# Optimization experiments

Hardware: AMD Instinct MI355X
Metric: run time of the kernel (lower is better)

## Reference

```python
import jax, jax.numpy as jnp
import numpy as np

N_NODES = 100000
N_EDGES = 640000
IN_DIM = 64
HID = 128
NUM_GRAPHS = 128
MPNN_STEPS = 3
S2S_STEPS = 3


def setup_inputs() -> dict:
    key = jax.random.key(0)
    ks = jax.random.split(key, 20)
    x = jax.random.normal(ks[0], (N_NODES, IN_DIM), dtype=jnp.float32)
    edge_index = jax.random.randint(ks[1], (2, N_EDGES), 0, N_NODES, dtype=jnp.int32)
    batch = jnp.sort(jax.random.randint(ks[2], (N_NODES,), 0, NUM_GRAPHS, dtype=jnp.int32))
    s = 1.0 / np.sqrt(HID)
    params = {
        # input layer Linear(64 -> 128)
        'W_in': jax.random.normal(ks[3], (HID, IN_DIM), dtype=jnp.float32) * s,
        'b_in': jax.random.normal(ks[4], (HID,), dtype=jnp.float32) * s,
        # MGU parameters (torch.randn init in source)
        'W_f': jax.random.normal(ks[5], (HID, HID), dtype=jnp.float32),
        'U_f': jax.random.normal(ks[6], (HID, HID), dtype=jnp.float32),
        'b_f': jax.random.normal(ks[7], (HID,), dtype=jnp.float32),
        'W_h': jax.random.normal(ks[8], (HID, HID), dtype=jnp.float32),
        'U_h': jax.random.normal(ks[9], (HID, HID), dtype=jnp.float32),
        'b_h': jax.random.normal(ks[10], (HID,), dtype=jnp.float32),
        # Set2Set LSTM: input 2*HID, hidden HID, gate order i,f,g,o
        'lstm_w_ih': jax.random.normal(ks[11], (4 * HID, 2 * HID), dtype=jnp.float32) * s,
        'lstm_w_hh': jax.random.normal(ks[12], (4 * HID, HID), dtype=jnp.float32) * s,
        'lstm_b_ih': jax.random.normal(ks[13], (4 * HID,), dtype=jnp.float32) * s,
        'lstm_b_hh': jax.random.normal(ks[14], (4 * HID,), dtype=jnp.float32) * s,
        # prediction layer Linear(2*HID -> 1)
        'W_pred': jax.random.normal(ks[15], (1, 2 * HID), dtype=jnp.float32) * s,
        'b_pred': jax.random.normal(ks[16], (1,), dtype=jnp.float32) * s,
    }
    return {'x': x, 'edge_index': edge_index, 'batch': batch, **params}


def _mpnn_mgu(h, src, dst, W_f, U_f, b_f, W_h, U_h, b_h):
    # sum-aggregate neighbor messages: m_i = sum_{j->i} h_j
    m = jax.ops.segment_sum(h[src], dst, num_segments=N_NODES)  # [N, H]
    f_t = jax.nn.sigmoid(m @ W_f.T + h @ U_f.T + b_f)
    h_hat = jnp.tanh(m @ W_h.T + (f_t * h) @ U_h.T + b_h)
    return (1.0 - f_t) * h + f_t * h_hat


def _set2set(x, batch, w_ih, w_hh, b_ih, b_hh):
    G, H = NUM_GRAPHS, HID
    q_star = jnp.zeros((G, 2 * H), dtype=x.dtype)
    h_l = jnp.zeros((G, H), dtype=x.dtype)
    c_l = jnp.zeros((G, H), dtype=x.dtype)
    for _ in range(S2S_STEPS):
        gates = q_star @ w_ih.T + h_l @ w_hh.T + b_ih + b_hh  # [G, 4H]
        i, f, g, o = jnp.split(gates, 4, axis=-1)
        c_l = jax.nn.sigmoid(f) * c_l + jax.nn.sigmoid(i) * jnp.tanh(g)
        h_l = jax.nn.sigmoid(o) * jnp.tanh(c_l)
        q = h_l  # [G, H]
        # attention over nodes within each graph segment
        e = jnp.sum(x * q[batch], axis=-1)  # [N]
        e_max = jax.ops.segment_max(e, batch, num_segments=G)
        a_un = jnp.exp(e - e_max[batch])
        denom = jax.ops.segment_sum(a_un, batch, num_segments=G)
        a = a_un / denom[batch]
        r = jax.ops.segment_sum(a[:, None] * x, batch, num_segments=G)  # [G, H]
        q_star = jnp.concatenate([q, r], axis=-1)
    return q_star


def reference(x, edge_index, batch, W_in, b_in, W_f, U_f, b_f, W_h, U_h, b_h,
              lstm_w_ih, lstm_w_hh, lstm_b_ih, lstm_b_hh, W_pred, b_pred):
    h = jax.nn.relu(x @ W_in.T + b_in)  # [N, HID]
    src, dst = edge_index[0], edge_index[1]
    for _ in range(MPNN_STEPS):
        h = _mpnn_mgu(h, src, dst, W_f, U_f, b_f, W_h, U_h, b_h)
    q_star = _set2set(h, batch, lstm_w_ih, lstm_w_hh, lstm_b_ih, lstm_b_hh)  # [G, 2H]
    return q_star @ W_pred.T + b_pred  # [G, 1]
```

## Files before the change

### kernel.cpp

```cpp
#include <hip/hip_runtime.h>
#include <math.h>

#define N_NODES 100000
#define N_EDGES 640000
#define IN_DIM 64
#define HID 128
#define NGRAPH 128

typedef __bf16 bf16x2 __attribute__((ext_vector_type(2)));
typedef __bf16 bf16x4 __attribute__((ext_vector_type(4)));
typedef __bf16 bf16x8 __attribute__((ext_vector_type(8)));
typedef float f32x4 __attribute__((ext_vector_type(4)));

#define LDST 136
#define KCAT 384
#define KPAD 392

__device__ __forceinline__ float sigmoid_f(float z) {
  return __fdividef(1.f, 1.f + __expf(-z));
}
__device__ __forceinline__ float tanh_f(float z) {
  return 1.f - __fdividef(2.f, __expf(2.f * z) + 1.f);
}

__device__ __forceinline__ void fma44(const float4 A[4], const float4 B[4], float acc[4][4]) {
#pragma unroll
  for (int i2 = 0; i2 < 4; ++i2) {
    acc[i2][0] += A[i2].x*B[0].x + A[i2].y*B[1].x + A[i2].z*B[2].x + A[i2].w*B[3].x;
    acc[i2][1] += A[i2].x*B[0].y + A[i2].y*B[1].y + A[i2].z*B[2].y + A[i2].w*B[3].y;
    acc[i2][2] += A[i2].x*B[0].z + A[i2].y*B[1].z + A[i2].z*B[2].z + A[i2].w*B[3].z;
    acc[i2][3] += A[i2].x*B[0].w + A[i2].y*B[1].w + A[i2].z*B[2].w + A[i2].w*B[3].w;
  }
}

__global__ __launch_bounds__(256) void k_input(const float* __restrict__ x,
                                               const float* __restrict__ W,
                                               const float* __restrict__ b,
                                               float* __restrict__ h) {
  __shared__ float wS[64][132];
  __shared__ float xS[32][68];
  int t = threadIdx.x;
  int nb = blockIdx.x * 32;
#pragma unroll
  for (int i = 0; i < 8; ++i) {
    int idx4 = i * 256 + t;
    int j = idx4 >> 4, kq = idx4 & 15;
    float4 v = ((const float4*)W)[j * 16 + kq];
    wS[4*kq+0][j] = v.x; wS[4*kq+1][j] = v.y; wS[4*kq+2][j] = v.z; wS[4*kq+3][j] = v.w;
  }
#pragma unroll
  for (int i = 0; i < 2; ++i) {
    int idx4 = i * 256 + t;
    int n = idx4 >> 4, kq = idx4 & 15;
    float4 v = ((const float4*)x)[(nb + n) * 16 + kq];
    *((float4*)&xS[n][4*kq]) = v;
  }
  __syncthreads();
  int bq = t & 31, a = t >> 5;
  float acc[4][4] = {};
#pragma unroll
  for (int kk4 = 0; kk4 < 16; ++kk4) {
    float4 A[4], B[4];
#pragma unroll
    for (int i2 = 0; i2 < 4; ++i2) A[i2] = *((const float4*)&xS[4*a+i2][4*kk4]);
#pragma unroll
    for (int c = 0; c < 4; ++c) B[c] = *((const float4*)&wS[4*kk4+c][4*bq]);
    fma44(A, B, acc);
  }
  float4 bb = ((const float4*)b)[bq];
  float ba[4] = {bb.x, bb.y, bb.z, bb.w};
#pragma unroll
  for (int i2 = 0; i2 < 4; ++i2) {
    float4 o;
    o.x = fmaxf(acc[i2][0] + ba[0], 0.f);
    o.y = fmaxf(acc[i2][1] + ba[1], 0.f);
    o.z = fmaxf(acc[i2][2] + ba[2], 0.f);
    o.w = fmaxf(acc[i2][3] + ba[3], 0.f);
    ((float4*)h)[(nb + 4*a + i2) * 32 + bq] = o;
  }
}

__global__ __launch_bounds__(256) void k_hist(const int* __restrict__ dst,
                                              int* __restrict__ deg) {
  int e = blockIdx.x * 256 + threadIdx.x;
  if (e < N_EDGES) atomicAdd(&deg[dst[e]], 1);
}

#define SCAN_CHUNK 4096
#define SCAN_NB 25

__global__ __launch_bounds__(256) void k_scan_part(const int* __restrict__ deg,
                                                   int* __restrict__ bsum) {
  __shared__ int red[256];
  int t = threadIdx.x, b = blockIdx.x;
  int base = b * SCAN_CHUNK + t * 16;
  int s = 0;
#pragma unroll
  for (int i = 0; i < 16; ++i) {
    int idx = base + i;
    if (idx < N_NODES) s += deg[idx];
  }
  red[t] = s;
  __syncthreads();
  for (int off = 128; off > 0; off >>= 1) {
    if (t < off) red[t] += red[t + off];
    __syncthreads();
  }
  if (t == 0) bsum[b] = red[0];
}

__global__ void k_scan_mid(const int* __restrict__ bsum, int* __restrict__ boff,
                           int* __restrict__ rowstart) {
  if (threadIdx.x == 0) {
    int run = 0;
    for (int i = 0; i < SCAN_NB; ++i) { boff[i] = run; run += bsum[i]; }
    rowstart[N_NODES] = run;
  }
}

__global__ __launch_bounds__(256) void k_scan_final(const int* __restrict__ deg,
                                                    const int* __restrict__ boff,
                                                    int* __restrict__ rowstart) {
  __shared__ int ts[256];
  int t = threadIdx.x, b = blockIdx.x;
  int base = b * SCAN_CHUNK + t * 16;
  int v[16];
  int s = 0;
#pragma unroll
  for (int i = 0; i < 16; ++i) {
    int idx = base + i;
    v[i] = (idx < N_NODES) ? deg[idx] : 0;
    s += v[i];
  }
  ts[t] = s;
  __syncthreads();
  for (int off = 1; off < 256; off <<= 1) {
    int add = (t >= off) ? ts[t - off] : 0;
    __syncthreads();
    ts[t] += add;
    __syncthreads();
  }
  int run = boff[b] + ts[t] - s;
#pragma unroll
  for (int i = 0; i < 16; ++i) {
    int idx = base + i;
    if (idx < N_NODES) rowstart[idx] = run;
    run += v[i];
  }
}

__global__ __launch_bounds__(256) void k_fill(const int* __restrict__ src,
                                              const int* __restrict__ dst,
                                              int* __restrict__ cursor,
                                              int* __restrict__ srcSorted) {
  int e = blockIdx.x * 256 + threadIdx.x;
  if (e >= N_EDGES) return;
  int d = dst[e];
  int p = atomicAdd(&cursor[d], 1);
  srcSorted[p] = src[e];
}

__global__ __launch_bounds__(256) void k_wsplit(const float* __restrict__ W0,
                                                const float* __restrict__ W1,
                                                const float* __restrict__ W2,
                                                const float* __restrict__ W3,
                                                __bf16* __restrict__ Whi,
                                                __bf16* __restrict__ Wlo) {
  int id = blockIdx.x * 256 + threadIdx.x;
  int mat = id >> 14, idx = id & 16383;
  const float* W = (mat == 0) ? W0 : (mat == 1) ? W1 : (mat == 2) ? W2 : W3;
  float v = W[idx];
  __bf16 hi = (__bf16)v;
  Whi[id] = hi;
  Wlo[id] = (__bf16)(v - (float)hi);
}

__global__ void k_wsplit2(const float* __restrict__ w_ih,
                          const float* __restrict__ w_hh,
                          __bf16* __restrict__ WcHi,
                          __bf16* __restrict__ WcLo) {
  int j = blockIdx.x;
  int k = threadIdx.x;
  float v = (k < 256) ? w_ih[j * 256 + k] : w_hh[j * 128 + (k - 256)];
  __bf16 hi = (__bf16)v;
  WcHi[j * KCAT + k] = hi;
  WcLo[j * KCAT + k] = (__bf16)(v - (float)hi);
}

__global__ __launch_bounds__(256) void k_gather(const float* __restrict__ h,
                                                const int* __restrict__ rowstart,
                                                const int* __restrict__ srcSorted,
                                                float* __restrict__ m) {
  int node = blockIdx.x * 8 + (threadIdx.x >> 5);
  if (node >= N_NODES) return;
  int li = threadIdx.x & 31;
  int j0 = rowstart[node], j1 = rowstart[node + 1];
  const float4* h4 = (const float4*)h;
  float4 a0 = {0.f, 0.f, 0.f, 0.f}, a1 = {0.f, 0.f, 0.f, 0.f};
  int j = j0;
  for (; j + 1 < j1; j += 2) {
    int s0 = srcSorted[j], s1 = srcSorted[j + 1];
    float4 v0 = h4[s0 * 32 + li];
    float4 v1 = h4[s1 * 32 + li];
    a0.x += v0.x; a0.y += v0.y; a0.z += v0.z; a0.w += v0.w;
    a1.x += v1.x; a1.y += v1.y; a1.z += v1.z; a1.w += v1.w;
  }
  if (j < j1) {
    int s0 = srcSorted[j];
    float4 v0 = h4[s0 * 32 + li];
    a0.x += v0.x; a0.y += v0.y; a0.z += v0.z; a0.w += v0.w;
  }
  float4 o = {a0.x + a1.x, a0.y + a1.y, a0.z + a1.z, a0.w + a1.w};
  ((float4*)m)[node * 32 + li] = o;
}

__global__ __launch_bounds__(256) void k_mgu(float* __restrict__ h,
                                             const float* __restrict__ m,
                                             const __bf16* __restrict__ Whi,
                                             const __bf16* __restrict__ Wlo,
                                             const float* __restrict__ bfp,
                                             const float* __restrict__ bhp) {
  __shared__ __bf16 mHi[64 * LDST], mLo[64 * LDST];
  __shared__ __bf16 hHi[64 * LDST], hLo[64 * LDST];
  const int t = threadIdx.x;
  const int nb = blockIdx.x * 64;

#pragma unroll
  for (int i = 0; i < 8; ++i) {
    int idx4 = i * 256 + t;
    int n = idx4 >> 5, kq = idx4 & 31;
    float4 vm = ((const float4*)m)[(nb + n) * 32 + kq];
    float4 vh = ((const float4*)h)[(nb + n) * 32 + kq];
    bf16x4 mh, ml, hh, hl;
    mh[0] = (__bf16)vm.x; ml[0] = (__bf16)(vm.x - (float)mh[0]);
    mh[1] = (__bf16)vm.y; ml[1] = (__bf16)(vm.y - (float)mh[1]);
    mh[2] = (__bf16)vm.z; ml[2] = (__bf16)(vm.z - (float)mh[2]);
    mh[3] = (__bf16)vm.w; ml[3] = (__bf16)(vm.w - (float)mh[3]);
    hh[0] = (__bf16)vh.x; hl[0] = (__bf16)(vh.x - (float)hh[0]);
    hh[1] = (__bf16)vh.y; hl[1] = (__bf16)(vh.y - (float)hh[1]);
    hh[2] = (__bf16)vh.z; hl[2] = (__bf16)(vh.z - (float)hh[2]);
    hh[3] = (__bf16)vh.w; hl[3] = (__bf16)(vh.w - (float)hh[3]);
    int e0 = n * LDST + 4 * kq;
    *(bf16x4*)&mHi[e0] = mh; *(bf16x4*)&mLo[e0] = ml;
    *(bf16x4*)&hHi[e0] = hh; *(bf16x4*)&hLo[e0] = hl;
  }
  __syncthreads();

  const int w = t >> 6, l = t & 63;
  const int lj = l & 15, q = l >> 4;

  float bfj[2], bhj[2];
#pragma unroll
  for (int ct = 0; ct < 2; ++ct) {
    int j = (2 * w + ct) * 16 + lj;
    bfj[ct] = bfp[j];
    bhj[ct] = bhp[j];
  }

  f32x4 acc[4][2] = {};

#pragma unroll
  for (int kc = 0; kc < 128; kc += 32) {
    bf16x8 bwh[2], bwl[2], buh[2], bul[2];
#pragma unroll
    for (int ct = 0; ct < 2; ++ct) {
      int off = ((2 * w + ct) * 16 + lj) * 128 + kc + q * 8;
      bwh[ct] = *(const bf16x8*)&Whi[off];
      bwl[ct] = *(const bf16x8*)&Wlo[off];
      buh[ct] = *(const bf16x8*)&Whi[16384 + off];
      bul[ct] = *(const bf16x8*)&Wlo[16384 + off];
    }
#pragma unroll
    for (int rt = 0; rt < 4; ++rt) {
      int e0 = (rt * 16 + lj) * LDST + kc + q * 8;
      bf16x8 amh = *(const bf16x8*)&mHi[e0];
      bf16x8 aml = *(const bf16x8*)&mLo[e0];
      bf16x8 ahh = *(const bf16x8*)&hHi[e0];
      bf16x8 ahl = *(const bf16x8*)&hLo[e0];
#pragma unroll
      for (int ct = 0; ct < 2; ++ct) {
        f32x4 a = acc[rt][ct];
        a = __builtin_amdgcn_mfma_f32_16x16x32_bf16(amh, bwh[ct], a, 0, 0, 0);
        a = __builtin_amdgcn_mfma_f32_16x16x32_bf16(amh, bwl[ct], a, 0, 0, 0);
        a = __builtin_amdgcn_mfma_f32_16x16x32_bf16(aml, bwh[ct], a, 0, 0, 0);
        a = __builtin_amdgcn_mfma_f32_16x16x32_bf16(ahh, buh[ct], a, 0, 0, 0);
        a = __builtin_amdgcn_mfma_f32_16x16x32_bf16(ahh, bul[ct], a, 0, 0, 0);
        a = __builtin_amdgcn_mfma_f32_16x16x32_bf16(ahl, buh[ct], a, 0, 0, 0);
        acc[rt][ct] = a;
      }
    }
  }

  __syncthreads();
  float fv[4][2][4], hvv[4][2][4];
#pragma unroll
  for (int rt = 0; rt < 4; ++rt)
#pragma unroll
    for (int ct = 0; ct < 2; ++ct) {
      int j = (2 * w + ct) * 16 + lj;
#pragma unroll
      for (int r = 0; r < 4; ++r) {
        int nl = rt * 16 + q * 4 + r;
        float z = acc[rt][ct][r] + bfj[ct];
        float f = sigmoid_f(z);
        int he = nl * LDST + j;
        float hval = (float)hHi[he] + (float)hLo[he];
        float g = f * hval;
        __bf16 ghi = (__bf16)g;
        hHi[he] = ghi;
        hLo[he] = (__bf16)(g - (float)ghi);
        fv[rt][ct][r] = f;
        hvv[rt][ct][r] = hval;
        acc[rt][ct][r] = 0.f;
      }
    }
  __syncthreads();

#pragma unroll
  for (int kc = 0; kc < 128; kc += 32) {
    bf16x8 bwh[2], bwl[2], buh[2], bul[2];
#pragma unroll
    for (int ct = 0; ct < 2; ++ct) {
      int off = ((2 * w + ct) * 16 + lj) * 128 + kc + q * 8;
      bwh[ct] = *(const bf16x8*)&Whi[2 * 16384 + off];
      bwl[ct] = *(const bf16x8*)&Wlo[2 * 16384 + off];
      buh[ct] = *(const bf16x8*)&Whi[3 * 16384 + off];
      bul[ct] = *(const bf16x8*)&Wlo[3 * 16384 + off];
    }
#pragma unroll
    for (int rt = 0; rt < 4; ++rt) {
      int e0 = (rt * 16 + lj) * LDST + kc + q * 8;
      bf16x8 amh = *(const bf16x8*)&mHi[e0];
      bf16x8 aml = *(const bf16x8*)&mLo[e0];
      bf16x8 agh = *(const bf16x8*)&hHi[e0];
      bf16x8 agl = *(const bf16x8*)&hLo[e0];
#pragma unroll
      for (int ct = 0; ct < 2; ++ct) {
        f32x4 a = acc[rt][ct];
        a = __builtin_amdgcn_mfma_f32_16x16x32_bf16(amh, bwh[ct], a, 0, 0, 0);
        a = __builtin_amdgcn_mfma_f32_16x16x32_bf16(amh, bwl[ct], a, 0, 0, 0);
        a = __builtin_amdgcn_mfma_f32_16x16x32_bf16(aml, bwh[ct], a, 0, 0, 0);
        a = __builtin_amdgcn_mfma_f32_16x16x32_bf16(agh, buh[ct], a, 0, 0, 0);
        a = __builtin_amdgcn_mfma_f32_16x16x32_bf16(agh, bul[ct], a, 0, 0, 0);
        a = __builtin_amdgcn_mfma_f32_16x16x32_bf16(agl, buh[ct], a, 0, 0, 0);
        acc[rt][ct] = a;
      }
    }
  }

#pragma unroll
  for (int rt = 0; rt < 4; ++rt)
#pragma unroll
    for (int ct = 0; ct < 2; ++ct) {
      int j = (2 * w + ct) * 16 + lj;
#pragma unroll
      for (int r = 0; r < 4; ++r) {
        float T = tanh_f(acc[rt][ct][r] + bhj[ct]);
        float f = fv[rt][ct][r];
        float hn = (1.f - f) * hvv[rt][ct][r] + f * T;
        h[(nb + rt * 16 + q * 4 + r) * 128 + j] = hn;
      }
    }
}

__global__ __launch_bounds__(256) void k_gates(const float* __restrict__ q_star,
                                               const float* __restrict__ h_l,
                                               const __bf16* __restrict__ WcHi,
                                               const __bf16* __restrict__ WcLo,
                                               float* __restrict__ gates) {
  __shared__ __bf16 sHi[64 * KPAD], sLo[64 * KPAD];
  const int t = threadIdx.x, b = blockIdx.x;
  const int w = t >> 6, l = t & 63, lj = l & 15, q = l >> 4;
  const int ct = b * 2 + (w & 1);
  const int rh = w >> 1;
  const float4* qs4 = (const float4*)q_star;
  const float4* hl4 = (const float4*)h_l;
  const int sg = t >> 2, part = t & 3;

  for (int chunk = 0; chunk < 2; ++chunk) {
    __syncthreads();
    int g0 = chunk * 64;
#pragma unroll
    for (int i = 0; i < 24; ++i) {
      int k4 = part * 24 + i;
      float4 v = (k4 < 64) ? qs4[(g0 + sg) * 64 + k4]
                           : hl4[(g0 + sg) * 32 + (k4 - 64)];
      bf16x4 hi, lo;
      hi[0] = (__bf16)v.x; lo[0] = (__bf16)(v.x - (float)hi[0]);
      hi[1] = (__bf16)v.y; lo[1] = (__bf16)(v.y - (float)hi[1]);
      hi[2] = (__bf16)v.z; lo[2] = (__bf16)(v.z - (float)hi[2]);
      hi[3] = (__bf16)v.w; lo[3] = (__bf16)(v.w - (float)hi[3]);
      int e0 = sg * KPAD + k4 * 4;
      *(bf16x4*)&sHi[e0] = hi; *(bf16x4*)&sLo[e0] = lo;
    }
    __syncthreads();
    f32x4 acc[2] = {};
#pragma unroll
    for (int kc = 0; kc < KCAT; kc += 32) {
      bf16x8 bh = *(const bf16x8*)&WcHi[(ct * 16 + lj) * KCAT + kc + q * 8];
      bf16x8 bl = *(const bf16x8*)&WcLo[(ct * 16 + lj) * KCAT + kc + q * 8];
#pragma unroll
      for (int rt = 0; rt < 2; ++rt) {
        int e0 = ((rh * 2 + rt) * 16 + lj) * KPAD + kc + q * 8;
        bf16x8 ah = *(const bf16x8*)&sHi[e0];
        bf16x8 al = *(const bf16x8*)&sLo[e0];
        f32x4 a = acc[rt];
        a = __builtin_amdgcn_mfma_f32_16x16x32_bf16(ah, bh, a, 0, 0, 0);
        a = __builtin_amdgcn_mfma_f32_16x16x32_bf16(ah, bl, a, 0, 0, 0);
        a = __builtin_amdgcn_mfma_f32_16x16x32_bf16(al, bh, a, 0, 0, 0);
        acc[rt] = a;
      }
    }
    int j = ct * 16 + lj;
#pragma unroll
    for (int rt = 0; rt < 2; ++rt)
#pragma unroll
      for (int r = 0; r < 4; ++r) {
        int g = g0 + (rh * 2 + rt) * 16 + q * 4 + r;
        gates[g * 512 + j] = acc[rt][r];
      }
  }
}

__global__ __launch_bounds__(256) void k_cell(const float* __restrict__ gates,
                                              const float* __restrict__ b_ih,
                                              const float* __restrict__ b_hh,
                                              float* __restrict__ q_star,
                                              float* __restrict__ h_l,
                                              float* __restrict__ c_l) {
  int id = blockIdx.x * 256 + threadIdx.x;
  int g = id >> 7, hu = id & 127;
  float gi = gates[g * 512 + hu]       + b_ih[hu]       + b_hh[hu];
  float gf = gates[g * 512 + 128 + hu] + b_ih[128 + hu] + b_hh[128 + hu];
  float gg = gates[g * 512 + 256 + hu] + b_ih[256 + hu] + b_hh[256 + hu];
  float go = gates[g * 512 + 384 + hu] + b_ih[384 + hu] + b_hh[384 + hu];
  float c = sigmoid_f(gf) * c_l[id] + sigmoid_f(gi) * tanh_f(gg);
  float hh = sigmoid_f(go) * tanh_f(c);
  c_l[id] = c;
  h_l[id] = hh;
  q_star[g * 256 + hu] = hh;
}

__global__ __launch_bounds__(1024) void k_attn(const float* __restrict__ h,
                                               const int* __restrict__ batch,
                                               float* __restrict__ q_star) {
  const int g = blockIdx.x, t = threadIdx.x;
  const int w = t >> 6, l = t & 63;
  const int half = l >> 5, li = l & 31;
  const int hw = 2 * w + half;
  __shared__ float redM[32], redS[32], scl[32];
  __shared__ float rPart[32][132];
  __shared__ float gInvS;
  __shared__ int bnd[2];

  if (t < 2) {
    int tgt = g + t;
    int lo = 0, hi = N_NODES;
    while (lo < hi) { int mid = (lo + hi) >> 1; if (batch[mid] < tgt) lo = mid + 1; else hi = mid; }
    bnd[t] = lo;
  }
  __syncthreads();
  const int s0 = bnd[0], s1 = bnd[1];

  float4 qv = ((const float4*)q_star)[g * 64 + li];
  const float q0 = qv.x, q1 = qv.y, q2 = qv.z, q3 = qv.w;

  float mw = -INFINITY, sw = 0.f;
  float4 racc = {0.f, 0.f, 0.f, 0.f};
  const float4* h4 = (const float4*)h;
  int n = s0 + hw;
  for (; n + 32 < s1; n += 64) {
    float4 hv0 = h4[n * 32 + li];
    float4 hv1 = h4[(n + 32) * 32 + li];
    float v0 = hv0.x * q0 + hv0.y * q1 + hv0.z * q2 + hv0.w * q3;
    float v1 = hv1.x * q0 + hv1.y * q1 + hv1.z * q2 + hv1.w * q3;
#pragma unroll
    for (int o = 16; o > 0; o >>= 1) {
      v0 += __shfl_xor(v0, o, 64);
      v1 += __shfl_xor(v1, o, 64);
    }
    float nm = fmaxf(mw, fmaxf(v0, v1));
    float sc = __expf(mw - nm);
    float w0 = __expf(v0 - nm);
    float w1 = __expf(v1 - nm);
    sw = sw * sc + w0 + w1;
    racc.x = racc.x * sc + w0 * hv0.x + w1 * hv1.x;
    racc.y = racc.y * sc + w0 * hv0.y + w1 * hv1.y;
    racc.z = racc.z * sc + w0 * hv0.z + w1 * hv1.z;
    racc.w = racc.w * sc + w0 * hv0.w + w1 * hv1.w;
    mw = nm;
  }
  for (; n < s1; n += 32) {
    float4 hv = h4[n * 32 + li];
    float v = hv.x * q0 + hv.y * q1 + hv.z * q2 + hv.w * q3;
#pragma unroll
    for (int o = 16; o > 0; o >>= 1) v += __shfl_xor(v, o, 64);
    float nm = fmaxf(mw, v);
    float sc = __expf(mw - nm);
    float wg = __expf(v - nm);
    sw = sw * sc + wg;
    racc.x = racc.x * sc + wg * hv.x;
    racc.y = racc.y * sc + wg * hv.y;
    racc.z = racc.z * sc + wg * hv.z;
    racc.w = racc.w * sc + wg * hv.w;
    mw = nm;
  }
  if (li == 0) { redM[hw] = mw; redS[hw] = sw; }
  *(float4*)&rPart[hw][4 * li] = racc;
  __syncthreads();
  if (t == 0) {
    float M = -INFINITY;
    for (int i = 0; i < 32; ++i) M = fmaxf(M, redM[i]);
    float S = 0.f;
    for (int i = 0; i < 32; ++i) {
      float s_ = (redM[i] > -INFINITY && M > -INFINITY) ? __expf(redM[i] - M) : 0.f;
      scl[i] = s_;
      S += redS[i] * s_;
    }
    gInvS = (S > 0.f) ? __fdividef(1.f, S) : 0.f;
  }
  __syncthreads();
  if (t < 128) {
    float inv = gInvS;
    float r = 0.f;
#pragma unroll
    for (int i = 0; i < 32; ++i) r += rPart[i][t] * scl[i];
    q_star[g * 256 + 128 + t] = r * inv;
  }
}

__global__ void k_pred(const float* __restrict__ q_star, const float* __restrict__ Wp,
                       const float* __restrict__ bp, float* __restrict__ out) {
  int g = threadIdx.x;
  float s = 0.f;
  for (int k = 0; k < 256; ++k) s += q_star[g * 256 + k] * Wp[k];
  out[g] = s + bp[0];
}

extern "C" void kernel_launch(void* const* d_in, const int* in_sizes, int n_in,
                              void* d_out, int out_size, void* d_ws, size_t ws_size,
                              hipStream_t stream) {
  const float* x      = (const float*)d_in[0];
  const int*   ei     = (const int*)d_in[1];
  const int*   batch  = (const int*)d_in[2];
  const float* W_in   = (const float*)d_in[3];
  const float* b_in   = (const float*)d_in[4];
  const float* W_f    = (const float*)d_in[5];
  const float* U_f    = (const float*)d_in[6];
  const float* b_f    = (const float*)d_in[7];
  const float* W_h    = (const float*)d_in[8];
  const float* U_h    = (const float*)d_in[9];
  const float* b_h    = (const float*)d_in[10];
  const float* w_ih   = (const float*)d_in[11];
  const float* w_hh   = (const float*)d_in[12];
  const float* b_ih   = (const float*)d_in[13];
  const float* b_hh   = (const float*)d_in[14];
  const float* W_pred = (const float*)d_in[15];
  const float* b_pred = (const float*)d_in[16];
  float* out = (float*)d_out;

  char* ws = (char*)d_ws;
  float* h      = (float*)(ws);
  float* m      = (float*)(ws + 51200000);
  int*   rowstart = (int*)(ws + 103063808);
  int*   srcSorted= (int*)(ws + 103463824);
  int*   bsum   = (int*)  (ws + 106023824);
  int*   boff   = (int*)  (ws + 106023936);
  int*    deg    = (int*)(ws + 102400000);
  int*    cursor = (int*)(ws + 102400000);
  __bf16* Whi    = (__bf16*)(ws + 102400000);
  __bf16* Wlo    = (__bf16*)(ws + 102531072);
  char* mB = (char*)m;
  __bf16* WcHi   = (__bf16*)(mB);
  __bf16* WcLo   = (__bf16*)(mB + 393216);
  float*  gates  = (float*)(mB + 786432);
  float*  q_star = (float*)(mB + 1048576);
  float*  h_l    = (float*)(mB + 1179648);
  float*  c_l    = (float*)(mB + 1245184);

  const int* src = ei;
  const int* dst = ei + N_EDGES;

  hipMemsetAsync(deg, 0, N_NODES * 4, stream);
  k_hist<<<(N_EDGES + 255) / 256, 256, 0, stream>>>(dst, deg);
  k_scan_part<<<SCAN_NB, 256, 0, stream>>>(deg, bsum);
  k_scan_mid<<<1, 32, 0, stream>>>(bsum, boff, rowstart);
  k_scan_final<<<SCAN_NB, 256, 0, stream>>>(deg, boff, rowstart);
  hipMemcpyAsync(cursor, rowstart, N_NODES * 4, hipMemcpyDeviceToDevice, stream);
  k_fill<<<(N_EDGES + 255) / 256, 256, 0, stream>>>(src, dst, cursor, srcSorted);

  k_wsplit<<<256, 256, 0, stream>>>(W_f, U_f, W_h, U_h, Whi, Wlo);

  k_input<<<N_NODES / 32, 256, 0, stream>>>(x, W_in, b_in, h);

  for (int step = 0; step < 3; ++step) {
    k_gather<<<(N_NODES + 7) / 8, 256, 0, stream>>>(h, rowstart, srcSorted, m);
    k_mgu<<<(N_NODES + 63) / 64, 256, 0, stream>>>(h, m, Whi, Wlo, b_f, b_h);
  }

  k_wsplit2<<<512, KCAT, 0, stream>>>(w_ih, w_hh, WcHi, WcLo);
  hipMemsetAsync(q_star, 0, 262144, stream);

  for (int s = 0; s < 3; ++s) {
    k_gates<<<16, 256, 0, stream>>>(q_star, h_l, WcHi, WcLo, gates);
    k_cell<<<64, 256, 0, stream>>>(gates, b_ih, b_hh, q_star, h_l, c_l);
    k_attn<<<NGRAPH, 1024, 0, stream>>>(h, batch, q_star);
  }

  k_pred<<<1, 128, 0, stream>>>(q_star, W_pred, b_pred, out);
}
```

Measured before the change: 729.6 us.

## Emit bf16 hi/lo split from gather and fuse LSTM gates with cell update

The gather kernel now writes the neighbor sum already split into bf16 hi/lo arrays, so the MGU kernel reads those operands straight from global memory. This drops the float m round trip and the per-block split and shared-memory staging of m, and it adds bounds clamping plus launch_bounds occupancy hint 4. The Set2Set gate GEMM and LSTM cell update are merged into one kernel with 8 blocks, each owning 16 hidden units across all four gates, which removes the gates buffer and one launch per step. In exchange, the MGU reads m fragments from global memory inside the MFMA loop, with somewhat uncoalesced bf16x8 loads, and the fused gates kernel runs with fewer blocks.

```diff
diff --git a/kernel.cpp b/kernel.cpp
--- a/kernel.cpp
+++ b/kernel.cpp
@@ -190,7 +190,8 @@
 __global__ __launch_bounds__(256) void k_gather(const float* __restrict__ h,
                                                 const int* __restrict__ rowstart,
                                                 const int* __restrict__ srcSorted,
-                                                float* __restrict__ m) {
+                                                __bf16* __restrict__ mHi,
+                                                __bf16* __restrict__ mLo) {
   int node = blockIdx.x * 8 + (threadIdx.x >> 5);
   if (node >= N_NODES) return;
   int li = threadIdx.x & 31;
@@ -211,16 +212,22 @@
     a0.x += v0.x; a0.y += v0.y; a0.z += v0.z; a0.w += v0.w;
   }
   float4 o = {a0.x + a1.x, a0.y + a1.y, a0.z + a1.z, a0.w + a1.w};
-  ((float4*)m)[node * 32 + li] = o;
-}
-
-__global__ __launch_bounds__(256) void k_mgu(float* __restrict__ h,
-                                             const float* __restrict__ m,
+  bf16x4 hi4, lo4;
+  hi4[0] = (__bf16)o.x; lo4[0] = (__bf16)(o.x - (float)hi4[0]);
+  hi4[1] = (__bf16)o.y; lo4[1] = (__bf16)(o.y - (float)hi4[1]);
+  hi4[2] = (__bf16)o.z; lo4[2] = (__bf16)(o.z - (float)hi4[2]);
+  hi4[3] = (__bf16)o.w; lo4[3] = (__bf16)(o.w - (float)hi4[3]);
+  ((bf16x4*)mHi)[node * 32 + li] = hi4;
+  ((bf16x4*)mLo)[node * 32 + li] = lo4;
+}
+
+__global__ __launch_bounds__(256, 4) void k_mgu(float* __restrict__ h,
+                                             const __bf16* __restrict__ mHi,
+                                             const __bf16* __restrict__ mLo,
                                              const __bf16* __restrict__ Whi,
                                              const __bf16* __restrict__ Wlo,
                                              const float* __restrict__ bfp,
                                              const float* __restrict__ bhp) {
-  __shared__ __bf16 mHi[64 * LDST], mLo[64 * LDST];
   __shared__ __bf16 hHi[64 * LDST], hLo[64 * LDST];
   const int t = threadIdx.x;
   const int nb = blockIdx.x * 64;
@@ -229,25 +236,27 @@
   for (int i = 0; i < 8; ++i) {
     int idx4 = i * 256 + t;
     int n = idx4 >> 5, kq = idx4 & 31;
-    float4 vm = ((const float4*)m)[(nb + n) * 32 + kq];
-    float4 vh = ((const float4*)h)[(nb + n) * 32 + kq];
-    bf16x4 mh, ml, hh, hl;
-    mh[0] = (__bf16)vm.x; ml[0] = (__bf16)(vm.x - (float)mh[0]);
-    mh[1] = (__bf16)vm.y; ml[1] = (__bf16)(vm.y - (float)mh[1]);
-    mh[2] = (__bf16)vm.z; ml[2] = (__bf16)(vm.z - (float)mh[2]);
-    mh[3] = (__bf16)vm.w; ml[3] = (__bf16)(vm.w - (float)mh[3]);
+    int row = nb + n; row = (row < N_NODES) ? row : (N_NODES - 1);
+    float4 vh = ((const float4*)h)[row * 32 + kq];
+    bf16x4 hh, hl;
     hh[0] = (__bf16)vh.x; hl[0] = (__bf16)(vh.x - (float)hh[0]);
     hh[1] = (__bf16)vh.y; hl[1] = (__bf16)(vh.y - (float)hh[1]);
     hh[2] = (__bf16)vh.z; hl[2] = (__bf16)(vh.z - (float)hh[2]);
     hh[3] = (__bf16)vh.w; hl[3] = (__bf16)(vh.w - (float)hh[3]);
     int e0 = n * LDST + 4 * kq;
-    *(bf16x4*)&mHi[e0] = mh; *(bf16x4*)&mLo[e0] = ml;
     *(bf16x4*)&hHi[e0] = hh; *(bf16x4*)&hLo[e0] = hl;
   }
   __syncthreads();
 
   const int w = t >> 6, l = t & 63;
   const int lj = l & 15, q = l >> 4;
+
+  int mrow[4];
+#pragma unroll
+  for (int rt = 0; rt < 4; ++rt) {
+    int r0 = nb + rt * 16 + lj;
+    mrow[rt] = (r0 < N_NODES) ? r0 : (N_NODES - 1);
+  }
 
   float bfj[2], bhj[2];
 #pragma unroll
@@ -272,9 +281,10 @@
     }
 #pragma unroll
     for (int rt = 0; rt < 4; ++rt) {
+      int mo = mrow[rt] * 128 + kc + q * 8;
+      bf16x8 amh = *(const bf16x8*)&mHi[mo];
+      bf16x8 aml = *(const bf16x8*)&mLo[mo];
       int e0 = (rt * 16 + lj) * LDST + kc + q * 8;
-      bf16x8 amh = *(const bf16x8*)&mHi[e0];
-      bf16x8 aml = *(const bf16x8*)&mLo[e0];
       bf16x8 ahh = *(const bf16x8*)&hHi[e0];
       bf16x8 ahl = *(const bf16x8*)&hLo[e0];
 #pragma unroll
@@ -329,9 +339,10 @@
     }
 #pragma unroll
     for (int rt = 0; rt < 4; ++rt) {
+      int mo = mrow[rt] * 128 + kc + q * 8;
+      bf16x8 amh = *(const bf16x8*)&mHi[mo];
+      bf16x8 aml = *(const bf16x8*)&mLo[mo];
       int e0 = (rt * 16 + lj) * LDST + kc + q * 8;
-      bf16x8 amh = *(const bf16x8*)&mHi[e0];
-      bf16x8 aml = *(const bf16x8*)&mLo[e0];
       bf16x8 agh = *(const bf16x8*)&hHi[e0];
       bf16x8 agl = *(const bf16x8*)&hLo[e0];
 #pragma unroll
@@ -355,27 +366,38 @@
       int j = (2 * w + ct) * 16 + lj;
 #pragma unroll
       for (int r = 0; r < 4; ++r) {
-        float T = tanh_f(acc[rt][ct][r] + bhj[ct]);
-        float f = fv[rt][ct][r];
-        float hn = (1.f - f) * hvv[rt][ct][r] + f * T;
-        h[(nb + rt * 16 + q * 4 + r) * 128 + j] = hn;
+        int row = nb + rt * 16 + q * 4 + r;
+        if (row < N_NODES) {
+          float T = tanh_f(acc[rt][ct][r] + bhj[ct]);
+          float f = fv[rt][ct][r];
+          float hn = (1.f - f) * hvv[rt][ct][r] + f * T;
+          h[row * 128 + j] = hn;
+        }
       }
     }
 }
 
-__global__ __launch_bounds__(256) void k_gates(const float* __restrict__ q_star,
-                                               const float* __restrict__ h_l,
-                                               const __bf16* __restrict__ WcHi,
-                                               const __bf16* __restrict__ WcLo,
-                                               float* __restrict__ gates) {
+__global__ __launch_bounds__(256) void k_gates_cell(float* __restrict__ q_star,
+                                                    float* __restrict__ h_l,
+                                                    float* __restrict__ c_l,
+                                                    const __bf16* __restrict__ WcHi,
+                                                    const __bf16* __restrict__ WcLo,
+                                                    const float* __restrict__ b_ih,
+                                                    const float* __restrict__ b_hh) {
   __shared__ __bf16 sHi[64 * KPAD], sLo[64 * KPAD];
   const int t = threadIdx.x, b = blockIdx.x;
   const int w = t >> 6, l = t & 63, lj = l & 15, q = l >> 4;
-  const int ct = b * 2 + (w & 1);
-  const int rh = w >> 1;
+  const int hu = b * 16 + lj;
   const float4* qs4 = (const float4*)q_star;
   const float4* hl4 = (const float4*)h_l;
   const int sg = t >> 2, part = t & 3;
+
+  float bs[4];
+#pragma unroll
+  for (int gt = 0; gt < 4; ++gt) {
+    int j = gt * 128 + hu;
+    bs[gt] = b_ih[j] + b_hh[j];
+  }
 
   for (int chunk = 0; chunk < 2; ++chunk) {
     __syncthreads();
@@ -394,51 +416,38 @@
       *(bf16x4*)&sHi[e0] = hi; *(bf16x4*)&sLo[e0] = lo;
     }
     __syncthreads();
-    f32x4 acc[2] = {};
+    f32x4 acc[4] = {};
 #pragma unroll
     for (int kc = 0; kc < KCAT; kc += 32) {
-      bf16x8 bh = *(const bf16x8*)&WcHi[(ct * 16 + lj) * KCAT + kc + q * 8];
-      bf16x8 bl = *(const bf16x8*)&WcLo[(ct * 16 + lj) * KCAT + kc + q * 8];
-#pragma unroll
-      for (int rt = 0; rt < 2; ++rt) {
-        int e0 = ((rh * 2 + rt) * 16 + lj) * KPAD + kc + q * 8;
-        bf16x8 ah = *(const bf16x8*)&sHi[e0];
-        bf16x8 al = *(const bf16x8*)&sLo[e0];
-        f32x4 a = acc[rt];
+      int e0 = (w * 16 + lj) * KPAD + kc + q * 8;
+      bf16x8 ah = *(const bf16x8*)&sHi[e0];
+      bf16x8 al = *(const bf16x8*)&sLo[e0];
+#pragma unroll
+      for (int gt = 0; gt < 4; ++gt) {
+        int off = (gt * 128 + hu) * KCAT + kc + q * 8;
+        bf16x8 bh = *(const bf16x8*)&WcHi[off];
+        bf16x8 bl = *(const bf16x8*)&WcLo[off];
+        f32x4 a = acc[gt];
         a = __builtin_amdgcn_mfma_f32_16x16x32_bf16(ah, bh, a, 0, 0, 0);
         a = __builtin_amdgcn_mfma_f32_16x16x32_bf16(ah, bl, a, 0, 0, 0);
         a = __builtin_amdgcn_mfma_f32_16x16x32_bf16(al, bh, a, 0, 0, 0);
-        acc[rt] = a;
+        acc[gt] = a;
       }
     }
-    int j = ct * 16 + lj;
-#pragma unroll
-    for (int rt = 0; rt < 2; ++rt)
-#pragma unroll
-      for (int r = 0; r < 4; ++r) {
-        int g = g0 + (rh * 2 + rt) * 16 + q * 4 + r;
-        gates[g * 512 + j] = acc[rt][r];
-      }
-  }
-}
-
-__global__ __launch_bounds__(256) void k_cell(const float* __restrict__ gates,
-                                              const float* __restrict__ b_ih,
-                                              const float* __restrict__ b_hh,
-                                              float* __restrict__ q_star,
-                                              float* __restrict__ h_l,
-                                              float* __restrict__ c_l) {
-  int id = blockIdx.x * 256 + threadIdx.x;
-  int g = id >> 7, hu = id & 127;
-  float gi = gates[g * 512 + hu]       + b_ih[hu]       + b_hh[hu];
-  float gf = gates[g * 512 + 128 + hu] + b_ih[128 + hu] + b_hh[128 + hu];
-  float gg = gates[g * 512 + 256 + hu] + b_ih[256 + hu] + b_hh[256 + hu];
-  float go = gates[g * 512 + 384 + hu] + b_ih[384 + hu] + b_hh[384 + hu];
-  float c = sigmoid_f(gf) * c_l[id] + sigmoid_f(gi) * tanh_f(gg);
-  float hh = sigmoid_f(go) * tanh_f(c);
-  c_l[id] = c;
-  h_l[id] = hh;
-  q_star[g * 256 + hu] = hh;
+#pragma unroll
+    for (int r = 0; r < 4; ++r) {
+      int g = g0 + w * 16 + q * 4 + r;
+      float zi = acc[0][r] + bs[0];
+      float zf = acc[1][r] + bs[1];
+      float zg = acc[2][r] + bs[2];
+      float zo = acc[3][r] + bs[3];
+      float c = sigmoid_f(zf) * c_l[g * 128 + hu] + sigmoid_f(zi) * tanh_f(zg);
+      float hh = sigmoid_f(zo) * tanh_f(c);
+      c_l[g * 128 + hu] = c;
+      h_l[g * 128 + hu] = hh;
+      q_star[g * 256 + hu] = hh;
+    }
+  }
 }
 
 __global__ __launch_bounds__(1024) void k_attn(const float* __restrict__ h,
@@ -560,8 +569,9 @@
   float* out = (float*)d_out;
 
   char* ws = (char*)d_ws;
-  float* h      = (float*)(ws);
-  float* m      = (float*)(ws + 51200000);
+  float*  h    = (float*)(ws);
+  __bf16* mHi  = (__bf16*)(ws + 51200000);
+  __bf16* mLo  = (__bf16*)(ws + 76800000);
   int*   rowstart = (int*)(ws + 103063808);
   int*   srcSorted= (int*)(ws + 103463824);
   int*   bsum   = (int*)  (ws + 106023824);
@@ -570,13 +580,12 @@
   int*    cursor = (int*)(ws + 102400000);
   __bf16* Whi    = (__bf16*)(ws + 102400000);
   __bf16* Wlo    = (__bf16*)(ws + 102531072);
-  char* mB = (char*)m;
-  __bf16* WcHi   = (__bf16*)(mB);
-  __bf16* WcLo   = (__bf16*)(mB + 393216);
-  float*  gates  = (float*)(mB + 786432);
-  float*  q_star = (float*)(mB + 1048576);
-  float*  h_l    = (float*)(mB + 1179648);
-  float*  c_l    = (float*)(mB + 1245184);
+  char* sB = (char*)srcSorted;
+  __bf16* WcHi   = (__bf16*)(sB);
+  __bf16* WcLo   = (__bf16*)(sB + 393216);
+  float*  q_star = (float*)(sB + 786432);
+  float*  h_l    = (float*)(sB + 917504);
+  float*  c_l    = (float*)(sB + 983040);
 
   const int* src = ei;
   const int* dst = ei + N_EDGES;
@@ -594,16 +603,15 @@
   k_input<<<N_NODES / 32, 256, 0, stream>>>(x, W_in, b_in, h);
 
   for (int step = 0; step < 3; ++step) {
-    k_gather<<<(N_NODES + 7) / 8, 256, 0, stream>>>(h, rowstart, srcSorted, m);
-    k_mgu<<<(N_NODES + 63) / 64, 256, 0, stream>>>(h, m, Whi, Wlo, b_f, b_h);
+    k_gather<<<(N_NODES + 7) / 8, 256, 0, stream>>>(h, rowstart, srcSorted, mHi, mLo);
+    k_mgu<<<(N_NODES + 63) / 64, 256, 0, stream>>>(h, mHi, mLo, Whi, Wlo, b_f, b_h);
   }
 
   k_wsplit2<<<512, KCAT, 0, stream>>>(w_ih, w_hh, WcHi, WcLo);
   hipMemsetAsync(q_star, 0, 262144, stream);
 
   for (int s = 0; s < 3; ++s) {
-    k_gates<<<16, 256, 0, stream>>>(q_star, h_l, WcHi, WcLo, gates);
-    k_cell<<<64, 256, 0, stream>>>(gates, b_ih, b_hh, q_star, h_l, c_l);
+    k_gates_cell<<<8, 256, 0, stream>>>(q_star, h_l, c_l, WcHi, WcLo, b_ih, b_hh);
     k_attn<<<NGRAPH, 1024, 0, stream>>>(h, batch, q_star);
   }
 
```

Result: slower. 1.015 ms (+39.1%).
